# Optimization experiments

Measured on AMD Instinct MI355X. Metric: run time of the kernel, lower is better.

Reference implementation:

```python
import jax, jax.numpy as jnp
import numpy as np

N_NODES = 100000
N_EDGES = 300000
N_GRAPHS = 512
D_IN = 256
D_HID = 256
D_OUT = 32


def setup_inputs() -> dict:
    key = jax.random.key(0)
    ks = jax.random.split(key, 12)
    x = jnp.zeros((N_NODES,), dtype=jnp.int64 if jax.config.jax_enable_x64 else jnp.int32)
    edge_index = jax.random.randint(ks[0], (2, N_EDGES), 0, N_NODES)
    batch = jnp.sort(jax.random.randint(ks[1], (N_NODES,), 0, N_GRAPHS))
    s_in = 1.0 / np.sqrt(D_IN)
    s_h = 1.0 / np.sqrt(D_HID)
    return {
        "x": x,
        "edge_index": edge_index,
        "batch": batch,
        "emb": jax.random.normal(ks[2], (1, D_IN), jnp.float32),
        "w1a": jax.random.normal(ks[3], (D_IN, D_HID), jnp.float32) * s_in,
        "b1a": jnp.zeros((D_HID,), jnp.float32),
        "w1b": jax.random.normal(ks[4], (D_HID, D_HID), jnp.float32) * s_h,
        "b1b": jnp.zeros((D_HID,), jnp.float32),
        "w2a": jax.random.normal(ks[5], (D_HID, D_HID), jnp.float32) * s_h,
        "b2a": jnp.zeros((D_HID,), jnp.float32),
        "w2b": jax.random.normal(ks[6], (D_HID, D_HID), jnp.float32) * s_h,
        "b2b": jnp.zeros((D_HID,), jnp.float32),
        "wf": jax.random.normal(ks[7], (D_HID, D_OUT), jnp.float32) * s_h,
        "bf": jnp.zeros((D_OUT,), jnp.float32),
    }


def _gin_conv(h, src, dst, wa, ba, wb, bb, num_nodes):
    # GINConv with default eps=0: mlp((1+eps)*h + sum_{j in N(i)} h_j)
    agg = jax.ops.segment_sum(h[src], dst, num_segments=num_nodes)
    z = h + agg
    z = jax.nn.relu(z @ wa + ba)
    return z @ wb + bb


def reference(x, edge_index, batch, emb, w1a, b1a, w1b, b1b,
              w2a, b2a, w2b, b2b, wf, bf):
    n = x.shape[0]
    src, dst = edge_index[0], edge_index[1]
    h = emb[x]                                  # [N, D_IN] embedding lookup
    h = _gin_conv(h, src, dst, w1a, b1a, w1b, b1b, n)
    h = jax.nn.relu(h)
    h = _gin_conv(h, src, dst, w2a, b2a, w2b, b2b, n)
    # global mean pool over graphs
    sums = jax.ops.segment_sum(h, batch, num_segments=N_GRAPHS)   # [G, D]
    counts = jax.ops.segment_sum(jnp.ones((n,), h.dtype), batch, num_segments=N_GRAPHS)
    pooled = sums / jnp.maximum(counts, 1.0)[:, None]
    return pooled @ wf + bf                     # [G, D_OUT]
```

## Files before the change

kernel.cpp:

```cpp
#include <hip/hip_runtime.h>
#include <cstddef>


#define BINS 32

typedef __attribute__((ext_vector_type(8))) short short8v;
typedef __attribute__((ext_vector_type(4))) float f32x4;

__device__ __forceinline__ int lower_bound(const int* __restrict__ b, int n, int v) {
    int lo = 0, hi = n;
    while (lo < hi) { int m = (lo + hi) >> 1; if (b[m] < v) lo = m + 1; else hi = m; }
    return lo;
}

__device__ __forceinline__ unsigned rne_bf16(float f) {
    unsigned u = __float_as_uint(f);
    return (u + 0x7FFFu + ((u >> 16) & 1u)) >> 16;
}

__global__ __launch_bounds__(256) void k_zero(float4* __restrict__ z, int n4) {
    int t = blockIdx.x * 256 + threadIdx.x;
    if (t < n4) z[t] = make_float4(0.f, 0.f, 0.f, 0.f);
}

__global__ __launch_bounds__(1024) void k_prep(
    const int* __restrict__ dst, unsigned* __restrict__ deg, int n_edges, int degb,
    const int* __restrict__ batch, int n_nodes, int n_graphs, int* __restrict__ gs0,
    float4* __restrict__ hz, int hz4,
    const float* __restrict__ emb, const float* __restrict__ w1a,
    const float* __restrict__ b1a, const float* __restrict__ w1b,
    const float* __restrict__ b1b, const float* __restrict__ w2a,
    unsigned short* __restrict__ Bpk,
    const float* __restrict__ w2b, const float* __restrict__ wf,
    const float* __restrict__ b2b, const float* __restrict__ bf,
    float* __restrict__ Wf2, float* __restrict__ bff,
    float* __restrict__ out) {
    __shared__ float pl[4][256];
    __shared__ float uv[256];
    const int tid = threadIdx.x;
    const int b = blockIdx.x;
    if (b < 32) {
        const int c = tid & 255, js = tid >> 8, d = b;
        const int j0 = js * 64;
        float p0 = 0.f, p1 = 0.f, p2 = 0.f, p3 = 0.f;
        for (int j = j0; j < j0 + 64; j += 4) {
            p0 += emb[j + 0] * w1a[(j + 0) * 256 + c];
            p1 += emb[j + 1] * w1a[(j + 1) * 256 + c];
            p2 += emb[j + 2] * w1a[(j + 2) * 256 + c];
            p3 += emb[j + 3] * w1a[(j + 3) * 256 + c];
        }
        pl[js][c] = (p0 + p1) + (p2 + p3);
        __syncthreads();
        if (js == 0) {
            float t0 = pl[0][c] + pl[1][c] + pl[2][c] + pl[3][c];
            uv[c] = fmaxf(fmaf((float)(1 + d), t0, b1a[c]), 0.f);
        }
        __syncthreads();
        p0 = p1 = p2 = p3 = 0.f;
        for (int j = j0; j < j0 + 64; j += 4) {
            p0 += uv[j + 0] * w1b[(j + 0) * 256 + c];
            p1 += uv[j + 1] * w1b[(j + 1) * 256 + c];
            p2 += uv[j + 2] * w1b[(j + 2) * 256 + c];
            p3 += uv[j + 3] * w1b[(j + 3) * 256 + c];
        }
        __syncthreads();
        pl[js][c] = (p0 + p1) + (p2 + p3);
        __syncthreads();
        if (js == 0) {
            float h1 = pl[0][c] + pl[1][c] + pl[2][c] + pl[3][c] + b1b[c];
            uv[c] = fmaxf(h1, 0.f);
        }
        __syncthreads();
        p0 = p1 = p2 = p3 = 0.f;
        for (int j = j0; j < j0 + 64; j += 4) {
            p0 += uv[j + 0] * w2a[(j + 0) * 256 + c];
            p1 += uv[j + 1] * w2a[(j + 1) * 256 + c];
            p2 += uv[j + 2] * w2a[(j + 2) * 256 + c];
            p3 += uv[j + 3] * w2a[(j + 3) * 256 + c];
        }
        pl[js][c] = (p0 + p1) + (p2 + p3);
        __syncthreads();
        if (js == 0) {
            const float yw = pl[0][c] + pl[1][c] + pl[2][c] + pl[3][c];
            const unsigned hb = rne_bf16(yw);
            const float hf = __uint_as_float(hb << 16);
            const unsigned lb = rne_bf16(yw - hf);
            const int tile = c >> 4;
            const int lane = ((d >> 3) << 4) | (c & 15);
            const int jj = d & 7;
            Bpk[((size_t)(0 * 16 + tile) * 64 + lane) * 8 + jj] = (unsigned short)hb;
            Bpk[((size_t)(1 * 16 + tile) * 64 + lane) * 8 + jj] = (unsigned short)lb;
        }
        return;
    }
    if (b < 40) {
        const int b2 = b - 32;
        const int k = b2 * 32 + (tid >> 5);
        const int o = tid & 31;
        float s = 0.f;
        for (int j = 0; j < 256; ++j) s += w2b[k * 256 + j] * wf[j * 32 + o];
        Wf2[k * 32 + o] = s;
        if (b2 == 0 && tid < 32) {
            float v = bf[o];
            for (int j = 0; j < 256; ++j) v += b2b[j] * wf[j * 32 + o];
            bff[o] = v;
        }
        return;
    }
    if (b == 40) {
        for (int t = tid; t <= n_graphs; t += 1024)
            gs0[t] = lower_bound(batch, n_nodes, t);
        __syncthreads();
        if (tid < n_graphs && gs0[tid + 1] == gs0[tid])
            for (int o = 0; o < 32; ++o) out[tid * 32 + o] = bf[o];
        return;
    }
    if (b < 41 + degb) {
        const int e = (b - 41) * 1024 + tid;
        if (e < n_edges) atomicAdd(&deg[dst[e]], 1u);
        return;
    }
    const int t = (b - 41 - degb) * 1024 + tid;
    if (t < hz4) hz[t] = make_float4(0.f, 0.f, 0.f, 0.f);
}

__global__ __launch_bounds__(256) void k_hist(const int* __restrict__ src,
                                              const int* __restrict__ dst,
                                              const unsigned* __restrict__ deg,
                                              unsigned* __restrict__ hist8, int n) {
    const int e = blockIdx.x * 256 + threadIdx.x;
    if (e < n) {
        const unsigned d = min(deg[src[e]], (unsigned)(BINS - 1));
        atomicAdd(&hist8[(size_t)dst[e] * 8 + (d >> 2)], 1u << (8 * (d & 3)));
    }
}

__global__ __launch_bounds__(256, 4) void k_gemm(const unsigned* __restrict__ hist8,
                                                 const unsigned* __restrict__ deg,
                                                 const int* __restrict__ batch,
                                                 const short8v* __restrict__ Bpk,
                                                 const float* __restrict__ b2a,
                                                 float* __restrict__ part,
                                                 int n_nodes) {
    __shared__ int s_c[2];
    const int tid = threadIdx.x;
    const int lane = tid & 63;
    const int wv = tid >> 6;
    const int blk = blockIdx.x;
    const int i0 = blk * 128;
    const int nn = min(128, n_nodes - i0);

    if (tid < 2) s_c[tid] = 0;
    __syncthreads();
    if (tid < 128) {
        const bool eq = (tid < nn) && (batch[i0 + tid] == batch[i0]);
        const unsigned long long m = __ballot(eq);
        if (lane == 0) s_c[wv] = __popcll(m);
    }
    __syncthreads();
    const int c0 = s_c[0], c1 = s_c[1];
    const int bnd = (c0 < min(nn, 64)) ? c0 : c0 + c1;

    short8v BH[4], BL[4];
    float b2af[4];
#pragma unroll
    for (int q = 0; q < 4; ++q) {
        BH[q] = Bpk[(0 * 16 + 4 * wv + q) * 64 + lane];
        BL[q] = Bpk[(1 * 16 + 4 * wv + q) * 64 + lane];
        b2af[q] = b2a[(4 * wv + q) * 16 + (lane & 15)];
    }
    float p0[4] = {0.f, 0.f, 0.f, 0.f};
    float p1[4] = {0.f, 0.f, 0.f, 0.f};

    const int ntiles = (nn + 15) >> 4;
    uint2 hh_n = make_uint2(0u, 0u);
    unsigned dg_n = 0u;
    if ((lane & 15) < nn) {
        const int node = i0 + (lane & 15);
        hh_n = *(const uint2*)(hist8 + (size_t)node * 8 + (lane >> 4) * 2);
        dg_n = deg[node];
    }
    for (int nt = 0; nt < ntiles; ++nt) {
        uint2 hh = hh_n;
        const unsigned dg = dg_n;
        const int offC = nt * 16 + (lane & 15);
        if (nt + 1 < ntiles) {
            const int offN = offC + 16;
            hh_n = make_uint2(0u, 0u); dg_n = 0u;
            if (offN < nn) {
                const int nodeN = i0 + offN;
                hh_n = *(const uint2*)(hist8 + (size_t)nodeN * 8 + (lane >> 4) * 2);
                dg_n = deg[nodeN];
            }
        }
        if (offC < nn) {
            const unsigned b0 = min(dg, (unsigned)(BINS - 1));
            if ((int)(b0 >> 3) == (lane >> 4)) {
                const unsigned bi = b0 & 7u;
                if (bi < 4) hh.x += 1u << (8 * bi);
                else        hh.y += 1u << (8 * (bi - 4));
            }
        }
        short8v A;
#pragma unroll
        for (int k = 0; k < 4; ++k) {
            const float f0 = (float)((hh.x >> (8 * k)) & 0xFFu);
            const float f1 = (float)((hh.y >> (8 * k)) & 0xFFu);
            A[k]     = (short)(__float_as_uint(f0) >> 16);
            A[k + 4] = (short)(__float_as_uint(f1) >> 16);
        }
        const int roff = nt * 16 + (lane >> 4) * 4;
#pragma unroll
        for (int q = 0; q < 4; ++q) {
            f32x4 acc = {0.f, 0.f, 0.f, 0.f};
            acc = __builtin_amdgcn_mfma_f32_16x16x32_bf16(A, BH[q], acc, 0, 0, 0);
            acc = __builtin_amdgcn_mfma_f32_16x16x32_bf16(A, BL[q], acc, 0, 0, 0);
#pragma unroll
            for (int j = 0; j < 4; ++j) {
                const int noff = roff + j;
                if (noff < nn) {
                    const float y = fmaxf(acc[j] + b2af[q], 0.f);
                    if (noff < bnd) p0[q] += y; else p1[q] += y;
                }
            }
        }
    }
#pragma unroll
    for (int q = 0; q < 4; ++q) {
        p0[q] += __shfl_xor(p0[q], 16); p0[q] += __shfl_xor(p0[q], 32);
        p1[q] += __shfl_xor(p1[q], 16); p1[q] += __shfl_xor(p1[q], 32);
    }
    if (lane < 16) {
        float* s0p = &part[(size_t)(2 * blk) * 256];
        float* s1p = &part[(size_t)(2 * blk + 1) * 256];
#pragma unroll
        for (int q = 0; q < 4; ++q) {
            s0p[(4 * wv + q) * 16 + lane] = p0[q];
            s1p[(4 * wv + q) * 16 + lane] = p1[q];
        }
    }
}

__global__ __launch_bounds__(256) void k_out(const int* __restrict__ batch,
                                             const int* __restrict__ gs0,
                                             const float* __restrict__ part,
                                             const float* __restrict__ Wf2,
                                             const float* __restrict__ bff,
                                             float* __restrict__ out, int n_graphs) {
    __shared__ float s_pool[256];
    __shared__ float s_red[256];
    const int g = blockIdx.x;
    const int tid = threadIdx.x;
    const int s0 = gs0[g];
    const int s1 = gs0[g + 1];
    if (s0 == s1) return;
    const float inv = 1.f / (float)(s1 - s0);
    float pc = 0.f;
    for (int w = s0 >> 7; w <= (s1 - 1) >> 7; ++w) {
        const int slot = 2 * w + (batch[w * 128] == g ? 0 : 1);
        pc += part[(size_t)slot * 256 + tid];
    }
    s_pool[tid] = pc * inv;
    __syncthreads();
    const int o = tid & 31, seg = tid >> 5;
    float sdot = 0.f;
    for (int c = seg * 32; c < seg * 32 + 32; ++c)
        sdot = fmaf(s_pool[c], Wf2[c * 32 + o], sdot);
    s_red[tid] = sdot;
    __syncthreads();
    if (tid < 32) {
        float r = bff[tid];
#pragma unroll
        for (int s = 0; s < 8; ++s) r += s_red[s * 32 + tid];
        out[g * 32 + tid] = r;
    }
}

extern "C" void kernel_launch(void* const* d_in, const int* in_sizes, int n_in,
                              void* d_out, int out_size, void* d_ws, size_t ws_size,
                              hipStream_t stream) {
    const int*   ei    = (const int*)d_in[1];
    const int*   batch = (const int*)d_in[2];
    const float* emb   = (const float*)d_in[3];
    const float* w1a   = (const float*)d_in[4];
    const float* b1a   = (const float*)d_in[5];
    const float* w1b   = (const float*)d_in[6];
    const float* b1b   = (const float*)d_in[7];
    const float* w2a   = (const float*)d_in[8];
    const float* b2a   = (const float*)d_in[9];
    const float* w2b   = (const float*)d_in[10];
    const float* b2b   = (const float*)d_in[11];
    const float* wf    = (const float*)d_in[12];
    const float* bf    = (const float*)d_in[13];

    const int n_nodes  = in_sizes[0];
    const int n_edges  = in_sizes[1] / 2;
    const int n_graphs = out_size / 32;
    const int* src = ei;
    const int* dst = ei + n_edges;
    const int nblocks = (n_nodes + 127) >> 7;

    char* wsp = (char*)d_ws;
    size_t off = 0;
    unsigned* hist8 = (unsigned*)(wsp + off); off += (size_t)n_nodes * 8 * 4;
    unsigned* deg   = (unsigned*)(wsp + off); off += (((size_t)n_nodes * 4) + 15) & ~(size_t)15;
    float*    part  = (float*)   (wsp + off); off += (size_t)2 * nblocks * 256 * 4;
    unsigned short* Bpk = (unsigned short*)(wsp + off); off += (size_t)2 * 16 * 64 * 8 * 2;
    float*    Wf2   = (float*)   (wsp + off); off += 256 * 32 * 4;
    float*    bff   = (float*)   (wsp + off); off += ((size_t)32 * 4 + 15) & ~(size_t)15;
    int*      gs0   = (int*)     (wsp + off); off += ((size_t)(n_graphs + 2) * 4 + 15) & ~(size_t)15;

    const size_t histB = (size_t)n_nodes * 8 * 4;
    const size_t degB  = (((size_t)n_nodes * 4) + 15) & ~(size_t)15;
    const int degn4 = (int)(degB / 16);
    const int hz4   = (int)(histB / 16);
    const int zb    = (hz4 + 1023) / 1024;
    const int degb  = (n_edges + 1023) / 1024;

    k_zero<<<(degn4 + 255) / 256, 256, 0, stream>>>((float4*)deg, degn4);
    k_prep<<<41 + degb + zb, 1024, 0, stream>>>(
        dst, deg, n_edges, degb, batch, n_nodes, n_graphs, gs0,
        (float4*)hist8, hz4,
        emb, w1a, b1a, w1b, b1b, w2a, Bpk,
        w2b, wf, b2b, bf, Wf2, bff, (float*)d_out);
    k_hist<<<(n_edges + 255) / 256, 256, 0, stream>>>(src, dst, deg, hist8, n_edges);
    k_gemm<<<nblocks, 256, 0, stream>>>(hist8, deg, batch, (const short8v*)Bpk,
                                        b2a, part, n_nodes);
    k_out<<<n_graphs, 256, 0, stream>>>(batch, gs0, part, Wf2, bff,
                                        (float*)d_out, n_graphs);
}
```

Baseline: 56.80 us.

## Reorder pipeline stages and batch-prefetch all histogram tiles in GEMM

Restructures the kernel sequence. One zero kernel now clears both the hist8 and deg buffers. A separate degree kernel follows, and the weight-prep work is merged with the histogram scatter in a single launch, so hist zeroing no longer shares a kernel with weight prep. The GEMM kernel now loads all eight 16-node tiles of hist8/deg into registers up front instead of using one-ahead prefetch, exposing more memory-level parallelism at the cost of extra registers. Launch count stays the same, but the histogram work is now co-scheduled with the weight precompute.

```diff
diff --git a/kernel.cpp b/kernel.cpp
--- a/kernel.cpp
+++ b/kernel.cpp
@@ -23,10 +23,16 @@
     if (t < n4) z[t] = make_float4(0.f, 0.f, 0.f, 0.f);
 }
 
-__global__ __launch_bounds__(1024) void k_prep(
-    const int* __restrict__ dst, unsigned* __restrict__ deg, int n_edges, int degb,
+__global__ __launch_bounds__(256) void k_deg(const int* __restrict__ dst,
+                                             unsigned* __restrict__ deg, int n) {
+    const int e = blockIdx.x * 256 + threadIdx.x;
+    if (e < n) atomicAdd(&deg[dst[e]], 1u);
+}
+
+__global__ __launch_bounds__(1024) void k_ph(
+    const int* __restrict__ src, const int* __restrict__ dst,
+    const unsigned* __restrict__ deg, unsigned* __restrict__ hist8, int n_edges,
     const int* __restrict__ batch, int n_nodes, int n_graphs, int* __restrict__ gs0,
-    float4* __restrict__ hz, int hz4,
     const float* __restrict__ emb, const float* __restrict__ w1a,
     const float* __restrict__ b1a, const float* __restrict__ w1b,
     const float* __restrict__ b1b, const float* __restrict__ w2a,
@@ -115,21 +121,8 @@
             for (int o = 0; o < 32; ++o) out[tid * 32 + o] = bf[o];
         return;
     }
-    if (b < 41 + degb) {
-        const int e = (b - 41) * 1024 + tid;
-        if (e < n_edges) atomicAdd(&deg[dst[e]], 1u);
-        return;
-    }
-    const int t = (b - 41 - degb) * 1024 + tid;
-    if (t < hz4) hz[t] = make_float4(0.f, 0.f, 0.f, 0.f);
-}
-
-__global__ __launch_bounds__(256) void k_hist(const int* __restrict__ src,
-                                              const int* __restrict__ dst,
-                                              const unsigned* __restrict__ deg,
-                                              unsigned* __restrict__ hist8, int n) {
-    const int e = blockIdx.x * 256 + threadIdx.x;
-    if (e < n) {
+    const int e = (b - 41) * 1024 + tid;
+    if (e < n_edges) {
         const unsigned d = min(deg[src[e]], (unsigned)(BINS - 1));
         atomicAdd(&hist8[(size_t)dst[e] * 8 + (d >> 2)], 1u << (8 * (d & 3)));
     }
@@ -173,39 +166,37 @@
     float p1[4] = {0.f, 0.f, 0.f, 0.f};
 
     const int ntiles = (nn + 15) >> 4;
-    uint2 hh_n = make_uint2(0u, 0u);
-    unsigned dg_n = 0u;
-    if ((lane & 15) < nn) {
-        const int node = i0 + (lane & 15);
-        hh_n = *(const uint2*)(hist8 + (size_t)node * 8 + (lane >> 4) * 2);
-        dg_n = deg[node];
-    }
-    for (int nt = 0; nt < ntiles; ++nt) {
-        uint2 hh = hh_n;
-        const unsigned dg = dg_n;
+    uint2 hh[8];
+    unsigned dgr[8];
+#pragma unroll
+    for (int nt = 0; nt < 8; ++nt) {
+        const int off = nt * 16 + (lane & 15);
+        hh[nt] = make_uint2(0u, 0u);
+        dgr[nt] = 0u;
+        if (nt < ntiles && off < nn) {
+            const int node = i0 + off;
+            hh[nt] = *(const uint2*)(hist8 + (size_t)node * 8 + (lane >> 4) * 2);
+            dgr[nt] = deg[node];
+        }
+    }
+#pragma unroll
+    for (int nt = 0; nt < 8; ++nt) {
+        if (nt >= ntiles) break;
+        uint2 h = hh[nt];
         const int offC = nt * 16 + (lane & 15);
-        if (nt + 1 < ntiles) {
-            const int offN = offC + 16;
-            hh_n = make_uint2(0u, 0u); dg_n = 0u;
-            if (offN < nn) {
-                const int nodeN = i0 + offN;
-                hh_n = *(const uint2*)(hist8 + (size_t)nodeN * 8 + (lane >> 4) * 2);
-                dg_n = deg[nodeN];
-            }
-        }
         if (offC < nn) {
-            const unsigned b0 = min(dg, (unsigned)(BINS - 1));
+            const unsigned b0 = min(dgr[nt], (unsigned)(BINS - 1));
             if ((int)(b0 >> 3) == (lane >> 4)) {
                 const unsigned bi = b0 & 7u;
-                if (bi < 4) hh.x += 1u << (8 * bi);
-                else        hh.y += 1u << (8 * (bi - 4));
+                if (bi < 4) h.x += 1u << (8 * bi);
+                else        h.y += 1u << (8 * (bi - 4));
             }
         }
         short8v A;
 #pragma unroll
         for (int k = 0; k < 4; ++k) {
-            const float f0 = (float)((hh.x >> (8 * k)) & 0xFFu);
-            const float f1 = (float)((hh.y >> (8 * k)) & 0xFFu);
+            const float f0 = (float)((h.x >> (8 * k)) & 0xFFu);
+            const float f1 = (float)((h.y >> (8 * k)) & 0xFFu);
             A[k]     = (short)(__float_as_uint(f0) >> 16);
             A[k + 4] = (short)(__float_as_uint(f1) >> 16);
         }
@@ -304,26 +295,23 @@
     size_t off = 0;
     unsigned* hist8 = (unsigned*)(wsp + off); off += (size_t)n_nodes * 8 * 4;
     unsigned* deg   = (unsigned*)(wsp + off); off += (((size_t)n_nodes * 4) + 15) & ~(size_t)15;
+    const size_t zeroB = off;
     float*    part  = (float*)   (wsp + off); off += (size_t)2 * nblocks * 256 * 4;
     unsigned short* Bpk = (unsigned short*)(wsp + off); off += (size_t)2 * 16 * 64 * 8 * 2;
     float*    Wf2   = (float*)   (wsp + off); off += 256 * 32 * 4;
     float*    bff   = (float*)   (wsp + off); off += ((size_t)32 * 4 + 15) & ~(size_t)15;
     int*      gs0   = (int*)     (wsp + off); off += ((size_t)(n_graphs + 2) * 4 + 15) & ~(size_t)15;
 
-    const size_t histB = (size_t)n_nodes * 8 * 4;
-    const size_t degB  = (((size_t)n_nodes * 4) + 15) & ~(size_t)15;
-    const int degn4 = (int)(degB / 16);
-    const int hz4   = (int)(histB / 16);
-    const int zb    = (hz4 + 1023) / 1024;
-    const int degb  = (n_edges + 1023) / 1024;
-
-    k_zero<<<(degn4 + 255) / 256, 256, 0, stream>>>((float4*)deg, degn4);
-    k_prep<<<41 + degb + zb, 1024, 0, stream>>>(
-        dst, deg, n_edges, degb, batch, n_nodes, n_graphs, gs0,
-        (float4*)hist8, hz4,
+    const int n4 = (int)(zeroB / 16);
+    const int histb = (n_edges + 1023) / 1024;
+
+    k_zero<<<(n4 + 255) / 256, 256, 0, stream>>>((float4*)d_ws, n4);
+    k_deg<<<(n_edges + 255) / 256, 256, 0, stream>>>(dst, deg, n_edges);
+    k_ph<<<41 + histb, 1024, 0, stream>>>(
+        src, dst, deg, hist8, n_edges,
+        batch, n_nodes, n_graphs, gs0,
         emb, w1a, b1a, w1b, b1b, w2a, Bpk,
         w2b, wf, b2b, bf, Wf2, bff, (float*)d_out);
-    k_hist<<<(n_edges + 255) / 256, 256, 0, stream>>>(src, dst, deg, hist8, n_edges);
     k_gemm<<<nblocks, 256, 0, stream>>>(hist8, deg, batch, (const short8v*)Bpk,
                                         b2a, part, n_nodes);
     k_out<<<n_graphs, 256, 0, stream>>>(batch, gs0, part, Wf2, bff,
```

Result: slower. 60.41 us (+6.3%).
